# Kernel optimization log

Hardware: AMD Instinct MI355X
Metric: run time of the kernel (lower is better)

Reference implementation:

```python
import jax, jax.numpy as jnp
import numpy as np

# Module hyperparameters (init_kwargs)
KH, KW = 1, 1            # kernel_size
PATCH_H, PATCH_W = 21, 21  # patch_size (displacement grid)
SH, SW = 1, 1            # stride
PAD_H, PAD_W = 0, 0      # padding
DILP_H, DILP_W = 1, 1    # dilation_patch
B, C, H, W = 8, 256, 64, 96


def setup_inputs() -> dict:
    key = jax.random.key(0)
    k1, k2 = jax.random.split(key)
    input1 = jax.random.normal(k1, (B, C, H, W), dtype=jnp.float32)
    input2 = jax.random.normal(k2, (B, C, H, W), dtype=jnp.float32)
    return {"input1": input1, "input2": input2}


def _correlation(x1, x2):
    """FlowNet-style spatial correlation (cost volume).

    out[b, pi, pj, i, j] = sum_{c, ki, kj}
        x1_pad[b, c, i*SH + ki, j*SW + kj] *
        x2_pad[b, c, i*SH + ki + (pi - radH)*DILP_H, j*SW + kj + (pj - radW)*DILP_W]
    Out-of-bounds reads of x2 are zero (handled by padding).
    """
    radH, radW = PATCH_H // 2, PATCH_W // 2
    x1p = jnp.pad(x1, ((0, 0), (0, 0), (PAD_H, PAD_H), (PAD_W, PAD_W)))
    x2p = jnp.pad(x2, ((0, 0), (0, 0),
                       (PAD_H + radH * DILP_H, PAD_H + radH * DILP_H),
                       (PAD_W + radW * DILP_W, PAD_W + radW * DILP_W)))
    Hp, Wp = H + 2 * PAD_H, W + 2 * PAD_W
    oH = (Hp - KH) // SH + 1
    oW = (Wp - KW) // SW + 1

    # displacement grid -> start offsets into x2p (0 corresponds to -rad shift)
    sh = jnp.arange(PATCH_H, dtype=jnp.int32) * DILP_H
    sw = jnp.arange(PATCH_W, dtype=jnp.int32) * DILP_W
    starts = jnp.stack(jnp.meshgrid(sh, sw, indexing="ij"), axis=-1).reshape(-1, 2)

    def step(carry, s):
        # shifted view of x2 aligned with padded x1
        sl = jax.lax.dynamic_slice(x2p, (0, 0, s[0], s[1]), (B, C, Hp, Wp))
        prod = jnp.sum(x1p * sl, axis=1)  # [B, Hp, Wp], channel reduction
        # kernel-window sum + output stride (KH=KW=1 -> single strided slice)
        acc = jnp.zeros((B, oH, oW), dtype=prod.dtype)
        for ki in range(KH):
            for kj in range(KW):
                acc = acc + jax.lax.slice(
                    prod, (0, ki, kj),
                    (B, ki + (oH - 1) * SH + 1, kj + (oW - 1) * SW + 1),
                    (1, SH, SW))
        return carry, acc

    _, out = jax.lax.scan(step, None, starts)  # [PATCH_H*PATCH_W, B, oH, oW]
    out = out.reshape(PATCH_H, PATCH_W, B, oH, oW)
    return jnp.transpose(out, (2, 0, 1, 3, 4))  # [B, patchH, patchW, oH, oW]


def reference(input1, input2):
    return _correlation(input1, input2)
```

## Files before the change

### kernel.cpp

```cpp
#include <hip/hip_runtime.h>

typedef __attribute__((ext_vector_type(8))) short short8;
typedef __attribute__((ext_vector_type(4))) float f32x4;
typedef __attribute__((ext_vector_type(4))) unsigned short us4;

constexpr int NB = 8, NC = 256, IH = 64, IW = 96;
constexpr int PATCH = 21, RAD = 10;
constexpr int TI = 8, TJ = 8;
constexpr int WIN = 28, NWIN = 784;
constexpr int KC = 32, NKS = NC / KC;
constexpr int PLANE = IH * IW;
constexpr int PH = IH + 2 * RAD, PW = IW + 2 * RAD;
constexpr int NBCH = NWIN * 4;
constexpr int NCHUNK = NBCH + 256;
constexpr int ASTR = IH * IW * KC;
constexpr int BSTR = PH * PW * KC;
constexpr size_t X1T_ELEMS = (size_t)NB * NKS * ASTR;
constexpr size_t X2P_ELEMS = (size_t)NB * NKS * BSTR;
constexpr int GSTR = 65;

__device__ __forceinline__ unsigned short f2bf(float f) {
  unsigned u = __builtin_bit_cast(unsigned, f);
  u += 0x7fffu + ((u >> 16) & 1u);
  return (unsigned short)(u >> 16);
}

__global__ __launch_bounds__(256) void x1_to_kmajor(
    const float* __restrict__ src, unsigned short* __restrict__ dst) {
  __shared__ float lsf[32 * 97];
  const int blk = blockIdx.x;
  const int ct = blk & 7, i = (blk >> 3) & 63, b = blk >> 9;
  const int c0 = ct * 32, t = threadIdx.x;
  const float* sp = src + ((size_t)b * NC + c0) * PLANE + (size_t)i * IW;
#pragma unroll
  for (int k = 0; k < 12; ++k) {
    int idx = k * 256 + t;
    int c = idx / 96, j = idx - c * 96;
    lsf[c * 97 + j] = sp[(size_t)c * PLANE + j];
  }
  __syncthreads();
  unsigned short* dp = dst + (((size_t)(b * NKS + ct) * IH + i) * IW) * KC;
#pragma unroll
  for (int k = 0; k < 3; ++k) {
    int o = k * 256 + t;
    int j = o >> 3, cq = o & 7;
    us4 v = {f2bf(lsf[(cq * 4 + 0) * 97 + j]), f2bf(lsf[(cq * 4 + 1) * 97 + j]),
             f2bf(lsf[(cq * 4 + 2) * 97 + j]), f2bf(lsf[(cq * 4 + 3) * 97 + j])};
    *(us4*)&dp[(size_t)j * KC + cq * 4] = v;
  }
}

__global__ __launch_bounds__(256) void x2_to_kmajor_pad(
    const float* __restrict__ src, unsigned short* __restrict__ dst) {
  __shared__ float lsf[32 * 97];
  const int blk = blockIdx.x;
  const int ct = blk & 7, i = (blk >> 3) % PH, b = blk / (PH * 8);
  const int c0 = ct * 32, t = threadIdx.x;
  const int isrc = i - RAD;
  const bool rowok = (unsigned)isrc < (unsigned)IH;
  if (rowok) {
    const float* sp = src + ((size_t)b * NC + c0) * PLANE + (size_t)isrc * IW;
#pragma unroll
    for (int k = 0; k < 12; ++k) {
      int idx = k * 256 + t;
      int c = idx / 96, j = idx - c * 96;
      lsf[c * 97 + j] = sp[(size_t)c * PLANE + j];
    }
  }
  __syncthreads();
  unsigned short* dp = dst + (((size_t)(b * NKS + ct) * PH + i) * PW) * KC;
#pragma unroll
  for (int k = 0; k < 4; ++k) {
    int o = k * 256 + t;
    if (o < PW * 8) {
      int j = o >> 3, cq = o & 7;
      int jsrc = j - RAD;
      us4 v = {0, 0, 0, 0};
      if (rowok && (unsigned)jsrc < (unsigned)IW)
        v = us4{f2bf(lsf[(cq * 4 + 0) * 97 + jsrc]), f2bf(lsf[(cq * 4 + 1) * 97 + jsrc]),
                f2bf(lsf[(cq * 4 + 2) * 97 + jsrc]), f2bf(lsf[(cq * 4 + 3) * 97 + jsrc])};
      *(us4*)&dp[(size_t)j * KC + cq * 4] = v;
    }
  }
}

__global__ __launch_bounds__(512, 2) void corr_pipe8(
    const unsigned short* __restrict__ x1k, const unsigned short* __restrict__ x2k,
    float* __restrict__ out) {
  __shared__ __attribute__((aligned(16))) unsigned short ls[3 * NCHUNK * 8];

  const int t = threadIdx.x, lane = t & 63, wv = t >> 6;
  const int bid = blockIdx.x;
  const int b = bid & 7;
  const int tile = bid >> 3;
  const int ti = tile / 12, tj = tile - ti * 12;
  const int i0 = ti * TI, j0 = tj * TJ;
  const int cbeg = 6 * wv;
  const int qk = lane >> 4, lr = lane & 15;

  const unsigned short* x1b = x1k + (size_t)b * NKS * ASTR;
  const unsigned short* x2b = x2k + (size_t)b * NKS * BSTR;

  const unsigned short* srcp[7];
#pragma unroll
  for (int it = 0; it < 7; ++it) {
    int q = it * 512 + t;
    if (q < NBCH) {
      int w = ((q >> 3) << 1) | (((q >> 2) ^ (q >> 4)) & 1);
      int c4 = (q & 3) ^ (w & 3);
      int wi = w / WIN, wj = w - wi * WIN;
      srcp[it] = x2b + ((size_t)(i0 + wi) * PW + (j0 + wj)) * KC + c4 * 8;
    } else {
      int qa = (q - NBCH) & 255;
      int m = ((qa >> 3) << 1) | (((qa >> 2) ^ (qa >> 4)) & 1);
      int c4 = (qa & 3) ^ (m & 3);
      srcp[it] = x1b + ((size_t)(i0 + (m >> 3)) * IW + (j0 + (m & 7))) * KC + c4 * 8;
    }
  }

  f32x4 acc[4][7];
#pragma unroll
  for (int a = 0; a < 4; ++a)
#pragma unroll
    for (int cc = 0; cc < 7; ++cc) acc[a][cc] = (f32x4){0.f, 0.f, 0.f, 0.f};

#define STAGE(BUF, KS)                                                              \
  {                                                                                 \
    unsigned short* lb = &ls[(BUF) * NCHUNK * 8];                                   \
    _Pragma("unroll")                                                               \
    for (int it = 0; it < 6; ++it)                                                  \
      __builtin_amdgcn_global_load_lds(                                             \
          (const void*)(srcp[it] + (size_t)(KS) * BSTR),                            \
          (void*)(lb + (it * 512 + wv * 64) * 8), 16, 0, 0);                        \
    if (wv < 5)                                                                     \
      __builtin_amdgcn_global_load_lds(                                             \
          (const void*)(srcp[6] + (size_t)(KS) * (wv == 0 ? BSTR : ASTR)),          \
          (void*)(lb + (3072 + wv * 64) * 8), 16, 0, 0);                            \
  }

#define COMPUTE(BUF)                                                                \
  {                                                                                 \
    const unsigned short* lb = &ls[(BUF) * NCHUNK * 8];                             \
    short8 af0 = *(const short8*)(lb + (NBCH + ((4 * (lr) + qk) ^ (lr & 7))) * 8);        \
    short8 af1 = *(const short8*)(lb + (NBCH + ((4 * (16 + lr) + qk) ^ (lr & 7))) * 8);   \
    short8 af2 = *(const short8*)(lb + (NBCH + ((4 * (32 + lr) + qk) ^ (lr & 7))) * 8);   \
    short8 af3 = *(const short8*)(lb + (NBCH + ((4 * (48 + lr) + qk) ^ (lr & 7))) * 8);   \
    _Pragma("unroll")                                                               \
    for (int cc = 0; cc < 7; ++cc) {                                                \
      int wrow = 16 * (cbeg + cc) + lr;                                             \
      int slot = (4 * wrow + qk) ^ (lr & 7);                                        \
      short8 bf = *(const short8*)(lb + slot * 8);                                  \
      acc[0][cc] = __builtin_amdgcn_mfma_f32_16x16x32_bf16(af0, bf, acc[0][cc], 0, 0, 0); \
      acc[1][cc] = __builtin_amdgcn_mfma_f32_16x16x32_bf16(af1, bf, acc[1][cc], 0, 0, 0); \
      acc[2][cc] = __builtin_amdgcn_mfma_f32_16x16x32_bf16(af2, bf, acc[2][cc], 0, 0, 0); \
      acc[3][cc] = __builtin_amdgcn_mfma_f32_16x16x32_bf16(af3, bf, acc[3][cc], 0, 0, 0); \
    }                                                                               \
  }

  STAGE(0, 0)
  STAGE(1, 1)

#define ITER(KS, VM)                                           \
  if ((KS) < 6) STAGE(((KS) + 2) % 3, (KS) + 2)                \
  asm volatile("s_waitcnt vmcnt(" #VM ")" ::: "memory");       \
  asm volatile("s_barrier" ::: "memory");                      \
  COMPUTE((KS) % 3)                                            \
  asm volatile("s_barrier" ::: "memory");

  ITER(0, 12)
  ITER(1, 12)
  ITER(2, 12)
  ITER(3, 12)
  ITER(4, 12)
  ITER(5, 12)
  ITER(6, 6)
  ITER(7, 0)
#undef ITER
#undef COMPUTE
#undef STAGE

  float* gf = (float*)ls;
#pragma unroll
  for (int ch = 0; ch < 2; ++ch) {
    __syncthreads();
    const int n0 = ch ? 384 : 0;
#pragma unroll
    for (int a = 0; a < 4; ++a)
#pragma unroll
      for (int cc = 0; cc < 7; ++cc) {
        int ccg = cbeg + cc;
        if (ch ? (ccg >= 24) : (ccg <= 24)) {
          int nl = 16 * ccg + lr - n0;
          int sm = 4 * a + qk;
          float* gp = &gf[nl * GSTR + 4 * (sm ^ (lr & 7))];
          gp[0] = acc[a][cc][0]; gp[1] = acc[a][cc][1];
          gp[2] = acc[a][cc][2]; gp[3] = acc[a][cc][3];
        }
      }
    __syncthreads();
    for (int s = t; s < 1764; s += 512) {
      int pidx = s / 21, pj = s - pidx * 21;
      int ii = 0, rem = pidx, stop = 0;
#pragma unroll
      for (int k = 0; k < 7; ++k) {
        int cnt = ch ? (7 + k) : (14 - k);
        int go = (!stop) && (rem >= cnt);
        rem -= go ? cnt : 0;
        ii += go;
        stop |= !go;
      }
      int pi = ch ? (14 - ii + rem) : rem;
      int nl = 28 * (pi + ii) + pj - n0;
      int ms = 8 * ii;
      float g[8];
#pragma unroll
      for (int e = 0; e < 8; ++e) {
        int m = ms + e, row = nl + e;
        g[e] = gf[row * GSTR + 4 * ((m >> 2) ^ (row & 7)) + (m & 3)];
      }
      float* op = out + ((((size_t)b * PATCH + pi) * PATCH + pj) * IH + (i0 + ii)) * IW + j0;
      f32x4 v0 = {g[0], g[1], g[2], g[3]};
      f32x4 v1 = {g[4], g[5], g[6], g[7]};
      *(f32x4*)op = v0;
      *(f32x4*)(op + 4) = v1;
    }
  }
}

constexpr int LDKF = 40;
__global__ __launch_bounds__(512, 2) void corr_mfma_fb(
    const float* __restrict__ x1, const float* __restrict__ x2, float* __restrict__ out) {
  __shared__ __attribute__((aligned(16))) unsigned short lsA[64 * LDKF];
  __shared__ __attribute__((aligned(16))) unsigned short lsB[NWIN * LDKF];
  const int t = threadIdx.x;
  const int b = blockIdx.y;
  const int ti = blockIdx.x / 12, tj = blockIdx.x % 12;
  const int i0 = ti * TI, j0 = tj * TJ;
  const int lane = t & 63, wv = t >> 6;
  const int mtp = wv >> 2, cg = wv & 3, cbeg = cg * 12;
  const int qk = lane >> 4, lr = lane & 15;
  f32x4 acc[2][13];
#pragma unroll
  for (int a = 0; a < 2; ++a)
#pragma unroll
    for (int cc = 0; cc < 13; ++cc) acc[a][cc] = (f32x4){0.f, 0.f, 0.f, 0.f};
  const int am = t & 63, ak4 = t >> 6;
  const int aii = am >> 3, ajj = am & 7;
  const float* x1p = x1 + ((size_t)b * NC + 4 * ak4) * PLANE + (size_t)(i0 + aii) * IW + (j0 + ajj);
  const float* x2b = x2 + (size_t)b * NC * PLANE;
  for (int ks = 0; ks < NKS; ++ks) {
    __syncthreads();
    {
      const float* p = x1p + (size_t)ks * KC * PLANE;
      us4 v = {f2bf(p[0]), f2bf(p[PLANE]), f2bf(p[2 * PLANE]), f2bf(p[3 * PLANE])};
      *(us4*)&lsA[am * LDKF + 4 * ak4] = v;
    }
    for (int w = t; w < NWIN; w += 512) {
      const int wi = w / WIN, wj = w - wi * WIN;
      const int gi = i0 - RAD + wi, gj = j0 - RAD + wj;
      const bool ok = ((unsigned)gi < (unsigned)IH) && ((unsigned)gj < (unsigned)IW);
      const float* p = x2b + ((size_t)(ks * KC) * IH + gi) * IW + gj;
      unsigned short* dst = &lsB[w * LDKF];
#pragma unroll
      for (int k4 = 0; k4 < 8; ++k4) {
        const float* q = p + (size_t)(4 * k4) * PLANE;
        us4 v = {f2bf(ok ? q[0] : 0.f), f2bf(ok ? q[PLANE] : 0.f),
                 f2bf(ok ? q[2 * PLANE] : 0.f), f2bf(ok ? q[3 * PLANE] : 0.f)};
        *(us4*)&dst[4 * k4] = v;
      }
    }
    __syncthreads();
    short8 a0 = *(const short8*)&lsA[(32 * mtp + lr) * LDKF + 8 * qk];
    short8 a1 = *(const short8*)&lsA[(32 * mtp + 16 + lr) * LDKF + 8 * qk];
#pragma unroll
    for (int cc = 0; cc < 13; ++cc) {
      const int wrow = 16 * (cbeg + cc) + lr;
      short8 bf = *(const short8*)&lsB[wrow * LDKF + 8 * qk];
      acc[0][cc] = __builtin_amdgcn_mfma_f32_16x16x32_bf16(a0, bf, acc[0][cc], 0, 0, 0);
      acc[1][cc] = __builtin_amdgcn_mfma_f32_16x16x32_bf16(a1, bf, acc[1][cc], 0, 0, 0);
    }
  }
#pragma unroll
  for (int a = 0; a < 2; ++a) {
    const int mb = 16 * (2 * mtp + a) + qk * 4;
#pragma unroll
    for (int cc = 0; cc < 13; ++cc) {
      if (cg > 0 && cc == 0) continue;
      const int n = 16 * (cbeg + cc) + lr;
      const int wi = n / WIN, wj = n - wi * WIN;
#pragma unroll
      for (int r = 0; r < 4; ++r) {
        const int m = mb + r;
        const int ii = m >> 3, jj = m & 7;
        const int pi = wi - ii, pj = wj - jj;
        if ((unsigned)pi < (unsigned)PATCH && (unsigned)pj < (unsigned)PATCH)
          out[((((size_t)b * PATCH + pi) * PATCH + pj) * IH + (i0 + ii)) * IW + (j0 + jj)] =
              acc[a][cc][r];
      }
    }
  }
}

extern "C" void kernel_launch(void* const* d_in, const int* in_sizes, int n_in,
                              void* d_out, int out_size, void* d_ws, size_t ws_size,
                              hipStream_t stream) {
  const float* x1 = (const float*)d_in[0];
  const float* x2 = (const float*)d_in[1];
  float* out = (float*)d_out;
  const size_t need = (X1T_ELEMS + X2P_ELEMS) * sizeof(unsigned short);
  if (ws_size >= need) {
    unsigned short* x1k = (unsigned short*)d_ws;
    unsigned short* x2k = x1k + X1T_ELEMS;
    x1_to_kmajor<<<NB * IH * 8, 256, 0, stream>>>(x1, x1k);
    x2_to_kmajor_pad<<<NB * PH * 8, 256, 0, stream>>>(x2, x2k);
    corr_pipe8<<<NB * 96, 512, 0, stream>>>(x1k, x2k, out);
  } else {
    dim3 grid(96, NB);
    corr_mfma_fb<<<grid, 512, 0, stream>>>(x1, x2, out);
  }
}
```

Before: 86.99 us.

## Retile correlation to 16-row x1 tiles split into half-window x2 blocks

```diff
diff --git a/kernel.cpp b/kernel.cpp
--- a/kernel.cpp
+++ b/kernel.cpp
@@ -6,18 +6,19 @@
 
 constexpr int NB = 8, NC = 256, IH = 64, IW = 96;
 constexpr int PATCH = 21, RAD = 10;
-constexpr int TI = 8, TJ = 8;
-constexpr int WIN = 28, NWIN = 784;
+constexpr int WIN = 28;
 constexpr int KC = 32, NKS = NC / KC;
 constexpr int PLANE = IH * IW;
 constexpr int PH = IH + 2 * RAD, PW = IW + 2 * RAD;
-constexpr int NBCH = NWIN * 4;
-constexpr int NCHUNK = NBCH + 256;
+constexpr int NPOS = 512;
+constexpr int NBCH = NPOS * 4;
+constexpr int NACH = 512;
+constexpr int NCHUNK = NBCH + NACH;
 constexpr int ASTR = IH * IW * KC;
 constexpr int BSTR = PH * PW * KC;
 constexpr size_t X1T_ELEMS = (size_t)NB * NKS * ASTR;
 constexpr size_t X2P_ELEMS = (size_t)NB * NKS * BSTR;
-constexpr int GSTR = 65;
+constexpr int GSTR = 129;
 
 __device__ __forceinline__ unsigned short f2bf(float f) {
   unsigned u = __builtin_bit_cast(unsigned, f);
@@ -84,7 +85,7 @@
   }
 }
 
-__global__ __launch_bounds__(512, 2) void corr_pipe8(
+__global__ __launch_bounds__(512, 2) void corr_half(
     const unsigned short* __restrict__ x1k, const unsigned short* __restrict__ x2k,
     float* __restrict__ out) {
   __shared__ __attribute__((aligned(16))) unsigned short ls[3 * NCHUNK * 8];
@@ -93,60 +94,61 @@
   const int bid = blockIdx.x;
   const int b = bid & 7;
   const int tile = bid >> 3;
-  const int ti = tile / 12, tj = tile - ti * 12;
-  const int i0 = ti * TI, j0 = tj * TJ;
-  const int cbeg = 6 * wv;
+  const int v = tile & 1;
+  const int tt = tile >> 1;
+  const int ti = tt / 12, tj = tt % 12;
+  const int i0 = 16 * ti, j0 = 8 * tj;
+  const int mg = wv >> 2;
+  const int cg = wv & 3;
+  const int cbeg = 8 * cg;
   const int qk = lane >> 4, lr = lane & 15;
 
   const unsigned short* x1b = x1k + (size_t)b * NKS * ASTR;
   const unsigned short* x2b = x2k + (size_t)b * NKS * BSTR;
 
-  const unsigned short* srcp[7];
-#pragma unroll
-  for (int it = 0; it < 7; ++it) {
+  const unsigned short* srcp[5];
+#pragma unroll
+  for (int it = 0; it < 5; ++it) {
     int q = it * 512 + t;
     if (q < NBCH) {
       int w = ((q >> 3) << 1) | (((q >> 2) ^ (q >> 4)) & 1);
       int c4 = (q & 3) ^ (w & 3);
-      int wi = w / WIN, wj = w - wi * WIN;
-      srcp[it] = x2b + ((size_t)(i0 + wi) * PW + (j0 + wj)) * KC + c4 * 8;
+      int wd = (w >= 504) ? (w - 504) : w;
+      int wi = wd / WIN, wj = wd - wi * WIN;
+      srcp[it] = x2b + ((size_t)(i0 + 18 * v + wi) * PW + (j0 + wj)) * KC + c4 * 8;
     } else {
-      int qa = (q - NBCH) & 255;
+      int qa = q - NBCH;
       int m = ((qa >> 3) << 1) | (((qa >> 2) ^ (qa >> 4)) & 1);
       int c4 = (qa & 3) ^ (m & 3);
       srcp[it] = x1b + ((size_t)(i0 + (m >> 3)) * IW + (j0 + (m & 7))) * KC + c4 * 8;
     }
   }
 
-  f32x4 acc[4][7];
+  f32x4 acc[4][8];
 #pragma unroll
   for (int a = 0; a < 4; ++a)
 #pragma unroll
-    for (int cc = 0; cc < 7; ++cc) acc[a][cc] = (f32x4){0.f, 0.f, 0.f, 0.f};
+    for (int cc = 0; cc < 8; ++cc) acc[a][cc] = (f32x4){0.f, 0.f, 0.f, 0.f};
 
 #define STAGE(BUF, KS)                                                              \
   {                                                                                 \
     unsigned short* lb = &ls[(BUF) * NCHUNK * 8];                                   \
     _Pragma("unroll")                                                               \
-    for (int it = 0; it < 6; ++it)                                                  \
+    for (int it = 0; it < 5; ++it)                                                  \
       __builtin_amdgcn_global_load_lds(                                             \
-          (const void*)(srcp[it] + (size_t)(KS) * BSTR),                            \
+          (const void*)(srcp[it] + (size_t)(KS) * (it < 4 ? BSTR : ASTR)),          \
           (void*)(lb + (it * 512 + wv * 64) * 8), 16, 0, 0);                        \
-    if (wv < 5)                                                                     \
-      __builtin_amdgcn_global_load_lds(                                             \
-          (const void*)(srcp[6] + (size_t)(KS) * (wv == 0 ? BSTR : ASTR)),          \
-          (void*)(lb + (3072 + wv * 64) * 8), 16, 0, 0);                            \
   }
 
 #define COMPUTE(BUF)                                                                \
   {                                                                                 \
     const unsigned short* lb = &ls[(BUF) * NCHUNK * 8];                             \
-    short8 af0 = *(const short8*)(lb + (NBCH + ((4 * (lr) + qk) ^ (lr & 7))) * 8);        \
-    short8 af1 = *(const short8*)(lb + (NBCH + ((4 * (16 + lr) + qk) ^ (lr & 7))) * 8);   \
-    short8 af2 = *(const short8*)(lb + (NBCH + ((4 * (32 + lr) + qk) ^ (lr & 7))) * 8);   \
-    short8 af3 = *(const short8*)(lb + (NBCH + ((4 * (48 + lr) + qk) ^ (lr & 7))) * 8);   \
+    short8 af0 = *(const short8*)(lb + (NBCH + ((64 * (4 * mg + 0) + 4 * lr + qk) ^ (lr & 7))) * 8); \
+    short8 af1 = *(const short8*)(lb + (NBCH + ((64 * (4 * mg + 1) + 4 * lr + qk) ^ (lr & 7))) * 8); \
+    short8 af2 = *(const short8*)(lb + (NBCH + ((64 * (4 * mg + 2) + 4 * lr + qk) ^ (lr & 7))) * 8); \
+    short8 af3 = *(const short8*)(lb + (NBCH + ((64 * (4 * mg + 3) + 4 * lr + qk) ^ (lr & 7))) * 8); \
     _Pragma("unroll")                                                               \
-    for (int cc = 0; cc < 7; ++cc) {                                                \
+    for (int cc = 0; cc < 8; ++cc) {                                                \
       int wrow = 16 * (cbeg + cc) + lr;                                             \
       int slot = (4 * wrow + qk) ^ (lr & 7);                                        \
       short8 bf = *(const short8*)(lb + slot * 8);                                  \
@@ -167,13 +169,13 @@
   COMPUTE((KS) % 3)                                            \
   asm volatile("s_barrier" ::: "memory");
 
-  ITER(0, 12)
-  ITER(1, 12)
-  ITER(2, 12)
-  ITER(3, 12)
-  ITER(4, 12)
-  ITER(5, 12)
-  ITER(6, 6)
+  ITER(0, 10)
+  ITER(1, 10)
+  ITER(2, 10)
+  ITER(3, 10)
+  ITER(4, 10)
+  ITER(5, 10)
+  ITER(6, 5)
   ITER(7, 0)
 #undef ITER
 #undef COMPUTE
@@ -181,41 +183,53 @@
 
   float* gf = (float*)ls;
 #pragma unroll
-  for (int ch = 0; ch < 2; ++ch) {
+  for (int p = 0; p < 2 + 1; ++p) {
     __syncthreads();
-    const int n0 = ch ? 384 : 0;
+    const int R0 = 168 * p;
 #pragma unroll
     for (int a = 0; a < 4; ++a)
 #pragma unroll
-      for (int cc = 0; cc < 7; ++cc) {
-        int ccg = cbeg + cc;
-        if (ch ? (ccg >= 24) : (ccg <= 24)) {
-          int nl = 16 * ccg + lr - n0;
-          int sm = 4 * a + qk;
-          float* gp = &gf[nl * GSTR + 4 * (sm ^ (lr & 7))];
+      for (int cc = 0; cc < 8; ++cc) {
+        int n = 16 * (cbeg + cc) + lr;
+        if (n >= R0 && n < R0 + 168) {
+          int rl = n - R0;
+          int sm = 4 * (4 * mg + a) + qk;
+          float* gp = &gf[rl * GSTR + 4 * (sm ^ (rl & 7))];
           gp[0] = acc[a][cc][0]; gp[1] = acc[a][cc][1];
           gp[2] = acc[a][cc][2]; gp[3] = acc[a][cc][3];
         }
       }
     __syncthreads();
-    for (int s = t; s < 1764; s += 512) {
+    int segs = 0;
+#pragma unroll
+    for (int kk = 0; kk < 6; ++kk) {
+      int W = 18 * v + 6 * p + kk;
+      int hi = W < 15 ? W : 15, lo = W - 20 > 0 ? W - 20 : 0;
+      segs += hi - lo + 1;
+    }
+    segs *= 21;
+    for (int s = t; s < segs; s += 512) {
       int pidx = s / 21, pj = s - pidx * 21;
-      int ii = 0, rem = pidx, stop = 0;
-#pragma unroll
-      for (int k = 0; k < 7; ++k) {
-        int cnt = ch ? (7 + k) : (14 - k);
-        int go = (!stop) && (rem >= cnt);
-        rem -= go ? cnt : 0;
-        ii += go;
+      int k = 0, rem = pidx, stop = 0;
+#pragma unroll
+      for (int kk = 0; kk < 5; ++kk) {
+        int W = 18 * v + 6 * p + kk;
+        int hi = W < 15 ? W : 15, lo = W - 20 > 0 ? W - 20 : 0;
+        int c = hi - lo + 1;
+        int go = (!stop) && (rem >= c);
+        rem -= go ? c : 0;
+        k += go;
         stop |= !go;
       }
-      int pi = ch ? (14 - ii + rem) : rem;
-      int nl = 28 * (pi + ii) + pj - n0;
-      int ms = 8 * ii;
+      int W = 18 * v + 6 * p + k;
+      int lo = W - 20 > 0 ? W - 20 : 0;
+      int ii = lo + rem;
+      int pi = W - ii;
+      int rl0 = 28 * k + pj;
       float g[8];
 #pragma unroll
       for (int e = 0; e < 8; ++e) {
-        int m = ms + e, row = nl + e;
+        int m = 8 * ii + e, row = rl0 + e;
         g[e] = gf[row * GSTR + 4 * ((m >> 2) ^ (row & 7)) + (m & 3)];
       }
       float* op = out + ((((size_t)b * PATCH + pi) * PATCH + pj) * IH + (i0 + ii)) * IW + j0;
@@ -228,14 +242,15 @@
 }
 
 constexpr int LDKF = 40;
+constexpr int NWINF = 784;
 __global__ __launch_bounds__(512, 2) void corr_mfma_fb(
     const float* __restrict__ x1, const float* __restrict__ x2, float* __restrict__ out) {
   __shared__ __attribute__((aligned(16))) unsigned short lsA[64 * LDKF];
-  __shared__ __attribute__((aligned(16))) unsigned short lsB[NWIN * LDKF];
+  __shared__ __attribute__((aligned(16))) unsigned short lsB[NWINF * LDKF];
   const int t = threadIdx.x;
   const int b = blockIdx.y;
   const int ti = blockIdx.x / 12, tj = blockIdx.x % 12;
-  const int i0 = ti * TI, j0 = tj * TJ;
+  const int i0 = ti * 8, j0 = tj * 8;
   const int lane = t & 63, wv = t >> 6;
   const int mtp = wv >> 2, cg = wv & 3, cbeg = cg * 12;
   const int qk = lane >> 4, lr = lane & 15;
@@ -255,7 +270,7 @@
       us4 v = {f2bf(p[0]), f2bf(p[PLANE]), f2bf(p[2 * PLANE]), f2bf(p[3 * PLANE])};
       *(us4*)&lsA[am * LDKF + 4 * ak4] = v;
     }
-    for (int w = t; w < NWIN; w += 512) {
+    for (int w = t; w < NWINF; w += 512) {
       const int wi = w / WIN, wj = w - wi * WIN;
       const int gi = i0 - RAD + wi, gj = j0 - RAD + wj;
       const bool ok = ((unsigned)gi < (unsigned)IH) && ((unsigned)gj < (unsigned)IW);
@@ -313,7 +328,7 @@
     unsigned short* x2k = x1k + X1T_ELEMS;
     x1_to_kmajor<<<NB * IH * 8, 256, 0, stream>>>(x1, x1k);
     x2_to_kmajor_pad<<<NB * PH * 8, 256, 0, stream>>>(x2, x2k);
-    corr_pipe8<<<NB * 96, 512, 0, stream>>>(x1k, x2k, out);
+    corr_half<<<NB * 96, 512, 0, stream>>>(x1k, x2k, out);
   } else {
     dim3 grid(96, NB);
     corr_mfma_fb<<<grid, 512, 0, stream>>>(x1, x2, out);
```

Result: no change. 87.73 us (+0.9%).
